# Kernel optimization log

Measured on AMD Instinct MI355X. Metric: run time of the kernel, lower is better.

## Reference

```python
import jax, jax.numpy as jnp
import numpy as np

N_SAMPLES = 9
N_FEATURES = 8
GRID_DIM = 200
H, W = 512, 512


def _corner_shifts():
    # same ordering as the torch module: i (x) outer, j (y), k (z) inner
    return jnp.array([[i, j, k] for i in (0, 1) for j in (0, 1) for k in (0, 1)], dtype=jnp.int32)


def setup_inputs() -> dict:
    key = jax.random.key(0)
    k1, k2, k3, k4 = jax.random.split(key, 4)
    b = 1
    vpoints = jax.random.uniform(k1, (b, H * W, 3), jnp.float32, 0.0, float(GRID_DIM))
    veye = jax.random.uniform(k2, (b, 3), jnp.float32, -float(GRID_DIM), 0.0)
    depth = jax.random.uniform(k3, (b, H, W), jnp.float32)
    grid = jax.random.normal(k4, (GRID_DIM, GRID_DIM, GRID_DIM, N_FEATURES), jnp.float32)
    empty_value = jnp.zeros((N_FEATURES,), jnp.float32)
    return {"vpoints": vpoints, "veye": veye, "depth": depth, "grid": grid, "empty_value": empty_value}


def _forward(vpoints, veye, depth, grid, empty_value):
    b, h, w = depth.shape
    # --- create_canonical_view: n_samples points along each viewing ray, centered on vpoints ---
    dirs = vpoints - veye[:, None, :]                                   # (b, n, 3)
    dirs = dirs / jnp.linalg.norm(dirs, axis=-1, keepdims=True)
    offs = jnp.arange(N_SAMPLES, dtype=vpoints.dtype) - (N_SAMPLES // 2)
    cv = vpoints[:, :, None, :] + offs[None, None, :, None] * dirs[:, :, None, :]  # (b, n, s, 3)
    points_normalized = cv - (jnp.floor(cv) + 0.5)

    pts = cv.reshape(-1, 3)  # b == 1 (original squeezes the batch dim); N = n*s
    xs, ys, zs, nf = grid.shape
    valid = ((pts[:, 0] >= 0) & (pts[:, 0] < xs)
             & (pts[:, 1] >= 0) & (pts[:, 1] < ys)
             & (pts[:, 2] >= 0) & (pts[:, 2] < zs))

    # replication-pad volume by 1 voxel; coords shifted by +1 into padded frame
    gp = jnp.pad(grid, ((1, 1), (1, 1), (1, 1), (0, 0)), mode="edge")
    p = jnp.where(valid[:, None], pts, 0.0) + 1.0   # invalid points mapped to a safe in-bounds index
    fl = jnp.floor(p)
    df = p - fl                                      # (N, 3) fractional offsets
    base = fl.astype(jnp.int32)
    idx = base[:, None, :] + _corner_shifts()[None]  # (N, 8, 3)

    corners = gp[idx[..., 0], idx[..., 1], idx[..., 2], :]  # (N, 8, nf) gather

    # trilinear weights, ordering matches corner shift ordering (4i + 2j + k)
    wx = jnp.stack([1.0 - df[:, 0], df[:, 0]], axis=1)
    wy = jnp.stack([1.0 - df[:, 1], df[:, 1]], axis=1)
    wz = jnp.stack([1.0 - df[:, 2], df[:, 2]], axis=1)
    wgt = (wx[:, :, None, None] * wy[:, None, :, None] * wz[:, None, None, :]).reshape(-1, 8)

    interp = jnp.einsum("nc,ncf->nf", wgt, corners)              # (N, nf)
    feats = jnp.where(valid[:, None], interp, empty_value[None, :])

    values = feats.reshape(b, h, w, N_SAMPLES * N_FEATURES)
    values = jnp.transpose(values, (0, 3, 1, 2))                 # (b, s*nf, h, w)
    return values, points_normalized, dirs


def reference(vpoints, veye, depth, grid, empty_value):
    return _forward(vpoints, veye, depth, grid, empty_value)
```

## Files before the change

### kernel.cpp

```cpp
#include <hip/hip_runtime.h>

#define HW (512 * 512)
#define GD 200
#define NS 9
#define NF 8
#define NPB 64
#define BT (NPB * NS)

__global__ __launch_bounds__(BT) void fusion_gather_kernel(
    const float* __restrict__ vpoints,
    const float* __restrict__ veye,
    const float* __restrict__ grid,
    const float* __restrict__ empty_value,
    float* __restrict__ out_values,
    float* __restrict__ out_pn,
    float* __restrict__ out_dirs)
{
    __shared__ float pnbuf[NPB * NS * 3];
    __shared__ float dirbuf[NPB * 3];

    int tid = threadIdx.x;
    int s = tid >> 6;
    int i = tid & 63;
    int n0 = blockIdx.x * NPB;
    int n = n0 + i;

    float px = vpoints[n * 3 + 0];
    float py = vpoints[n * 3 + 1];
    float pz = vpoints[n * 3 + 2];
    float ex = veye[0], ey = veye[1], ez = veye[2];

    float dx = px - ex, dy = py - ey, dz = pz - ez;
    float inv = 1.0f / sqrtf(dx * dx + dy * dy + dz * dz);
    dx *= inv; dy *= inv; dz *= inv;

    if (s == 4) {
        dirbuf[i * 3 + 0] = dx;
        dirbuf[i * 3 + 1] = dy;
        dirbuf[i * 3 + 2] = dz;
    }

    float off = (float)(s - NS / 2);
    float cx = px + off * dx;
    float cy = py + off * dy;
    float cz = pz + off * dz;

    pnbuf[i * 27 + s * 3 + 0] = cx - (floorf(cx) + 0.5f);
    pnbuf[i * 27 + s * 3 + 1] = cy - (floorf(cy) + 0.5f);
    pnbuf[i * 27 + s * 3 + 2] = cz - (floorf(cz) + 0.5f);

    bool valid = (cx >= 0.0f) && (cx < (float)GD) &&
                 (cy >= 0.0f) && (cy < (float)GD) &&
                 (cz >= 0.0f) && (cz < (float)GD);

    float ft[NF];
#pragma unroll
    for (int f = 0; f < NF; ++f) ft[f] = empty_value[f];

    const float4* g4 = (const float4*)grid;

    if (valid) {
        float p0 = cx + 1.0f, p1 = cy + 1.0f, p2 = cz + 1.0f;
        float f0 = floorf(p0), f1 = floorf(p1), f2 = floorf(p2);
        float d0 = p0 - f0, d1 = p1 - f1, d2 = p2 - f2;
        int bx = (int)f0, by = (int)f1, bz = (int)f2;
        int X0 = bx - 1, X1 = min(bx, GD - 1);
        int Y0 = by - 1, Y1 = min(by, GD - 1);
        int Z0 = bz - 1, Z1 = min(bz, GD - 1);

        float wz0 = 1.0f - d2, wz1 = d2;

        float acc[NF];
#pragma unroll
        for (int f = 0; f < NF; ++f) acc[f] = 0.0f;

#pragma unroll
        for (int ix = 0; ix < 2; ++ix) {
            int X = ix ? X1 : X0;
            float wx = ix ? d0 : (1.0f - d0);
#pragma unroll
            for (int iy = 0; iy < 2; ++iy) {
                int Y = iy ? Y1 : Y0;
                float wy = iy ? d1 : (1.0f - d1);
                float wxy = wx * wy;
                int rowbase = (X * GD + Y) * GD;
                float4 a0 = g4[(size_t)(rowbase + Z0) * 2 + 0];
                float4 a1 = g4[(size_t)(rowbase + Z0) * 2 + 1];
                float4 b0 = g4[(size_t)(rowbase + Z1) * 2 + 0];
                float4 b1 = g4[(size_t)(rowbase + Z1) * 2 + 1];
                float w0 = wxy * wz0, w1 = wxy * wz1;
                acc[0] += w0 * a0.x + w1 * b0.x;
                acc[1] += w0 * a0.y + w1 * b0.y;
                acc[2] += w0 * a0.z + w1 * b0.z;
                acc[3] += w0 * a0.w + w1 * b0.w;
                acc[4] += w0 * a1.x + w1 * b1.x;
                acc[5] += w0 * a1.y + w1 * b1.y;
                acc[6] += w0 * a1.z + w1 * b1.z;
                acc[7] += w0 * a1.w + w1 * b1.w;
            }
        }
#pragma unroll
        for (int f = 0; f < NF; ++f) ft[f] = acc[f];
    }

#pragma unroll
    for (int f = 0; f < NF; ++f)
        __builtin_nontemporal_store(ft[f], &out_values[(size_t)(s * NF + f) * HW + n]);

    __syncthreads();

    const size_t pn_base = (size_t)n0 * (NS * 3);
#pragma unroll
    for (int k = 0; k < 3; ++k) {
        int idx = tid + k * BT;
        __builtin_nontemporal_store(pnbuf[idx], &out_pn[pn_base + idx]);
    }
    if (tid < NPB * 3)
        __builtin_nontemporal_store(dirbuf[tid], &out_dirs[(size_t)n0 * 3 + tid]);
}

extern "C" void kernel_launch(void* const* d_in, const int* in_sizes, int n_in,
                              void* d_out, int out_size, void* d_ws, size_t ws_size,
                              hipStream_t stream) {
    const float* vpoints = (const float*)d_in[0];
    const float* veye = (const float*)d_in[1];
    const float* grid = (const float*)d_in[3];
    const float* empty_value = (const float*)d_in[4];

    float* out = (float*)d_out;
    float* out_values = out;
    float* out_pn = out + (size_t)NS * NF * HW;
    float* out_dirs = out_pn + (size_t)HW * NS * 3;

    dim3 block(BT);
    dim3 grid_dim(HW / NPB);
    hipLaunchKernelGGL(fusion_gather_kernel, grid_dim, block, 0, stream,
                       vpoints, veye, grid, empty_value,
                       out_values, out_pn, out_dirs);
}
```

Before: 187.3 us.

## Process two rays per thread with branchless clamped gathers for more memory parallelism

Each thread now handles two ray points (NPB doubled, block size unchanged), so two independent sets of eight-corner gathers are in flight per thread. The validity branch is removed: indices are clamped into range, loads always run, and the result is chosen with a select. The aim is to hide gather latency on the large grid through more memory-level parallelism. The cost is higher register pressure, half as many blocks, and wasted loads for invalid points.

```diff
diff --git a/kernel.cpp b/kernel.cpp
--- a/kernel.cpp
+++ b/kernel.cpp
@@ -4,10 +4,72 @@
 #define GD 200
 #define NS 9
 #define NF 8
-#define NPB 64
-#define BT (NPB * NS)
+#define NPB 128
+#define BT (64 * NS)
 
-__global__ __launch_bounds__(BT) void fusion_gather_kernel(
+__device__ __forceinline__ void ray_setup(
+    float px, float py, float pz, float ex, float ey, float ez, float off,
+    float& cx, float& cy, float& cz, float& dx, float& dy, float& dz)
+{
+    dx = px - ex; dy = py - ey; dz = pz - ez;
+    float inv = 1.0f / sqrtf(dx * dx + dy * dy + dz * dz);
+    dx *= inv; dy *= inv; dz *= inv;
+    cx = px + off * dx; cy = py + off * dy; cz = pz + off * dz;
+}
+
+__device__ __forceinline__ void addr_setup(
+    float cx, float cy, float cz,
+    int& X0, int& X1, int& Y0, int& Y1, int& Z0, int& Z1,
+    float& d0, float& d1, float& d2, bool& valid)
+{
+    valid = (cx >= 0.0f) && (cx < (float)GD) &&
+            (cy >= 0.0f) && (cy < (float)GD) &&
+            (cz >= 0.0f) && (cz < (float)GD);
+    float p0 = cx + 1.0f, p1 = cy + 1.0f, p2 = cz + 1.0f;
+    float f0 = floorf(p0), f1 = floorf(p1), f2 = floorf(p2);
+    d0 = p0 - f0; d1 = p1 - f1; d2 = p2 - f2;
+    int bx = (int)f0, by = (int)f1, bz = (int)f2;
+    X0 = min(max(bx - 1, 0), GD - 1); X1 = min(max(bx, 0), GD - 1);
+    Y0 = min(max(by - 1, 0), GD - 1); Y1 = min(max(by, 0), GD - 1);
+    Z0 = min(max(bz - 1, 0), GD - 1); Z1 = min(max(bz, 0), GD - 1);
+}
+
+__device__ __forceinline__ void gather8(
+    const float4* __restrict__ g4,
+    int X0, int X1, int Y0, int Y1, int Z0, int Z1,
+    float d0, float d1, float d2, float* acc)
+{
+    float wz0 = 1.0f - d2, wz1 = d2;
+#pragma unroll
+    for (int f = 0; f < NF; ++f) acc[f] = 0.0f;
+#pragma unroll
+    for (int ix = 0; ix < 2; ++ix) {
+        int X = ix ? X1 : X0;
+        float wx = ix ? d0 : (1.0f - d0);
+#pragma unroll
+        for (int iy = 0; iy < 2; ++iy) {
+            int Y = iy ? Y1 : Y0;
+            float wy = iy ? d1 : (1.0f - d1);
+            float wxy = wx * wy;
+            int rowbase = (X * GD + Y) * GD;
+            float4 a0 = g4[(size_t)(rowbase + Z0) * 2 + 0];
+            float4 a1 = g4[(size_t)(rowbase + Z0) * 2 + 1];
+            float4 b0 = g4[(size_t)(rowbase + Z1) * 2 + 0];
+            float4 b1 = g4[(size_t)(rowbase + Z1) * 2 + 1];
+            float w0 = wxy * wz0, w1 = wxy * wz1;
+            acc[0] += w0 * a0.x + w1 * b0.x;
+            acc[1] += w0 * a0.y + w1 * b0.y;
+            acc[2] += w0 * a0.z + w1 * b0.z;
+            acc[3] += w0 * a0.w + w1 * b0.w;
+            acc[4] += w0 * a1.x + w1 * b1.x;
+            acc[5] += w0 * a1.y + w1 * b1.y;
+            acc[6] += w0 * a1.z + w1 * b1.z;
+            acc[7] += w0 * a1.w + w1 * b1.w;
+        }
+    }
+}
+
+__global__ __launch_bounds__(BT, 4) void fusion_gather_kernel(
     const float* __restrict__ vpoints,
     const float* __restrict__ veye,
     const float* __restrict__ grid,
@@ -23,95 +85,61 @@
     int s = tid >> 6;
     int i = tid & 63;
     int n0 = blockIdx.x * NPB;
-    int n = n0 + i;
+    int nA = n0 + i;
+    int nB = n0 + 64 + i;
 
-    float px = vpoints[n * 3 + 0];
-    float py = vpoints[n * 3 + 1];
-    float pz = vpoints[n * 3 + 2];
     float ex = veye[0], ey = veye[1], ez = veye[2];
+    float off = (float)(s - NS / 2);
 
-    float dx = px - ex, dy = py - ey, dz = pz - ez;
-    float inv = 1.0f / sqrtf(dx * dx + dy * dy + dz * dz);
-    dx *= inv; dy *= inv; dz *= inv;
+    float pxA = vpoints[nA * 3 + 0], pyA = vpoints[nA * 3 + 1], pzA = vpoints[nA * 3 + 2];
+    float pxB = vpoints[nB * 3 + 0], pyB = vpoints[nB * 3 + 1], pzB = vpoints[nB * 3 + 2];
+
+    float cxA, cyA, czA, dxA, dyA, dzA;
+    float cxB, cyB, czB, dxB, dyB, dzB;
+    ray_setup(pxA, pyA, pzA, ex, ey, ez, off, cxA, cyA, czA, dxA, dyA, dzA);
+    ray_setup(pxB, pyB, pzB, ex, ey, ez, off, cxB, cyB, czB, dxB, dyB, dzB);
 
     if (s == 4) {
-        dirbuf[i * 3 + 0] = dx;
-        dirbuf[i * 3 + 1] = dy;
-        dirbuf[i * 3 + 2] = dz;
+        dirbuf[i * 3 + 0] = dxA; dirbuf[i * 3 + 1] = dyA; dirbuf[i * 3 + 2] = dzA;
+        dirbuf[(64 + i) * 3 + 0] = dxB; dirbuf[(64 + i) * 3 + 1] = dyB; dirbuf[(64 + i) * 3 + 2] = dzB;
     }
 
-    float off = (float)(s - NS / 2);
-    float cx = px + off * dx;
-    float cy = py + off * dy;
-    float cz = pz + off * dz;
+    pnbuf[i * 27 + s * 3 + 0] = cxA - (floorf(cxA) + 0.5f);
+    pnbuf[i * 27 + s * 3 + 1] = cyA - (floorf(cyA) + 0.5f);
+    pnbuf[i * 27 + s * 3 + 2] = czA - (floorf(czA) + 0.5f);
+    pnbuf[(64 + i) * 27 + s * 3 + 0] = cxB - (floorf(cxB) + 0.5f);
+    pnbuf[(64 + i) * 27 + s * 3 + 1] = cyB - (floorf(cyB) + 0.5f);
+    pnbuf[(64 + i) * 27 + s * 3 + 2] = czB - (floorf(czB) + 0.5f);
 
-    pnbuf[i * 27 + s * 3 + 0] = cx - (floorf(cx) + 0.5f);
-    pnbuf[i * 27 + s * 3 + 1] = cy - (floorf(cy) + 0.5f);
-    pnbuf[i * 27 + s * 3 + 2] = cz - (floorf(cz) + 0.5f);
-
-    bool valid = (cx >= 0.0f) && (cx < (float)GD) &&
-                 (cy >= 0.0f) && (cy < (float)GD) &&
-                 (cz >= 0.0f) && (cz < (float)GD);
-
-    float ft[NF];
-#pragma unroll
-    for (int f = 0; f < NF; ++f) ft[f] = empty_value[f];
+    int X0A, X1A, Y0A, Y1A, Z0A, Z1A;
+    int X0B, X1B, Y0B, Y1B, Z0B, Z1B;
+    float d0A, d1A, d2A, d0B, d1B, d2B;
+    bool vA, vB;
+    addr_setup(cxA, cyA, czA, X0A, X1A, Y0A, Y1A, Z0A, Z1A, d0A, d1A, d2A, vA);
+    addr_setup(cxB, cyB, czB, X0B, X1B, Y0B, Y1B, Z0B, Z1B, d0B, d1B, d2B, vB);
 
     const float4* g4 = (const float4*)grid;
+    float accA[NF], accB[NF];
+    gather8(g4, X0A, X1A, Y0A, Y1A, Z0A, Z1A, d0A, d1A, d2A, accA);
+    gather8(g4, X0B, X1B, Y0B, Y1B, Z0B, Z1B, d0B, d1B, d2B, accB);
 
-    if (valid) {
-        float p0 = cx + 1.0f, p1 = cy + 1.0f, p2 = cz + 1.0f;
-        float f0 = floorf(p0), f1 = floorf(p1), f2 = floorf(p2);
-        float d0 = p0 - f0, d1 = p1 - f1, d2 = p2 - f2;
-        int bx = (int)f0, by = (int)f1, bz = (int)f2;
-        int X0 = bx - 1, X1 = min(bx, GD - 1);
-        int Y0 = by - 1, Y1 = min(by, GD - 1);
-        int Z0 = bz - 1, Z1 = min(bz, GD - 1);
-
-        float wz0 = 1.0f - d2, wz1 = d2;
-
-        float acc[NF];
+    float ev[NF];
 #pragma unroll
-        for (int f = 0; f < NF; ++f) acc[f] = 0.0f;
+    for (int f = 0; f < NF; ++f) ev[f] = empty_value[f];
 
 #pragma unroll
-        for (int ix = 0; ix < 2; ++ix) {
-            int X = ix ? X1 : X0;
-            float wx = ix ? d0 : (1.0f - d0);
-#pragma unroll
-            for (int iy = 0; iy < 2; ++iy) {
-                int Y = iy ? Y1 : Y0;
-                float wy = iy ? d1 : (1.0f - d1);
-                float wxy = wx * wy;
-                int rowbase = (X * GD + Y) * GD;
-                float4 a0 = g4[(size_t)(rowbase + Z0) * 2 + 0];
-                float4 a1 = g4[(size_t)(rowbase + Z0) * 2 + 1];
-                float4 b0 = g4[(size_t)(rowbase + Z1) * 2 + 0];
-                float4 b1 = g4[(size_t)(rowbase + Z1) * 2 + 1];
-                float w0 = wxy * wz0, w1 = wxy * wz1;
-                acc[0] += w0 * a0.x + w1 * b0.x;
-                acc[1] += w0 * a0.y + w1 * b0.y;
-                acc[2] += w0 * a0.z + w1 * b0.z;
-                acc[3] += w0 * a0.w + w1 * b0.w;
-                acc[4] += w0 * a1.x + w1 * b1.x;
-                acc[5] += w0 * a1.y + w1 * b1.y;
-                acc[6] += w0 * a1.z + w1 * b1.z;
-                acc[7] += w0 * a1.w + w1 * b1.w;
-            }
-        }
-#pragma unroll
-        for (int f = 0; f < NF; ++f) ft[f] = acc[f];
+    for (int f = 0; f < NF; ++f) {
+        __builtin_nontemporal_store(vA ? accA[f] : ev[f],
+                                    &out_values[(size_t)(s * NF + f) * HW + nA]);
+        __builtin_nontemporal_store(vB ? accB[f] : ev[f],
+                                    &out_values[(size_t)(s * NF + f) * HW + nB]);
     }
-
-#pragma unroll
-    for (int f = 0; f < NF; ++f)
-        __builtin_nontemporal_store(ft[f], &out_values[(size_t)(s * NF + f) * HW + n]);
 
     __syncthreads();
 
     const size_t pn_base = (size_t)n0 * (NS * 3);
 #pragma unroll
-    for (int k = 0; k < 3; ++k) {
+    for (int k = 0; k < 6; ++k) {
         int idx = tid + k * BT;
         __builtin_nontemporal_store(pnbuf[idx], &out_pn[pn_base + idx]);
     }
```

Measured after the change: 200.7 us. +7.1%, slower.
